# Performance work log

Hardware: AMD Instinct MI355X
Metric: run time of the kernel (lower is better)

## Reference

```python
import jax, jax.numpy as jnp
import numpy as np

B, S, D, H = 4, 2048, 512, 8
HD = D // H  # 64


def setup_inputs() -> dict:
    key = jax.random.key(0)
    ks = jax.random.split(key, 7)
    scale = 1.0 / np.sqrt(D)
    return {
        "query": jax.random.normal(ks[0], (B, S, D), jnp.float32),
        "key": jax.random.normal(ks[1], (B, S, D), jnp.float32),
        "value": jax.random.normal(ks[2], (B, S, D), jnp.float32),
        # Only the `query` Linear and fc_out are actually used in the original forward
        "Wq": jax.random.uniform(ks[3], (D, D), jnp.float32, -scale, scale),
        "bq": jnp.zeros((D,), jnp.float32),
        "Wo": jax.random.uniform(ks[4], (D, D), jnp.float32, -scale, scale),
        "bo": jnp.zeros((D,), jnp.float32),
    }


def reference(query, key, value, Wq, bq, Wo, bo):
    # Faithful to source: Q, K, V all use the *query* projection (bug preserved)
    def proj(x):
        # [B,S,D] -> [B,H,S,HD]
        y = x @ Wq + bq
        return y.reshape(B, S, H, HD).transpose(0, 2, 1, 3)

    Q, K, V = proj(query), proj(key), proj(value)
    scores = jnp.einsum("bhqd,bhkd->bhqk", Q, K) / jnp.sqrt(jnp.float32(HD))
    attn = jax.nn.softmax(scores, axis=-1)
    x = jnp.einsum("bhqk,bhkd->bhqd", attn, V)
    x = x.transpose(0, 2, 1, 3).reshape(B, S, D)
    return x @ Wo + bo
```

## Files before the change

### kernel.cpp

```cpp
#include <hip/hip_runtime.h>
#include <math.h>

#define B_ 4
#define S_ 2048
#define D_ 512
#define H_ 8
#define HD_ 64
#define SZ_ (B_ * S_ * D_)
#define WSZ_ (D_ * D_)
#define BSH_ (B_ * S_ * H_)

#define QSCALE_ 0.18033688011112042f

typedef _Float16 v4h __attribute__((ext_vector_type(4)));
typedef _Float16 v8h __attribute__((ext_vector_type(8)));
typedef float    v4f __attribute__((ext_vector_type(4)));

#define GLD16(g, l)                                                         \
    __builtin_amdgcn_global_load_lds(                                       \
        (const __attribute__((address_space(1))) unsigned int*)(g),         \
        (__attribute__((address_space(3))) unsigned int*)(l), 16, 0, 0)

__global__ __launch_bounds__(256) void wtrans_kernel(const float* __restrict__ Wq,
                                                     const float* __restrict__ Wo,
                                                     _Float16* __restrict__ Wt) {
    __shared__ float Ts[64][65];
    const float* W = blockIdx.z ? Wo : Wq;
    _Float16* dst = Wt + (size_t)blockIdx.z * WSZ_;
    const int t = threadIdx.x;
    const int k0 = blockIdx.y * 64, n0 = blockIdx.x * 64;
#pragma unroll
    for (int i = 0; i < 4; i++) {
        int c = t + i * 256;
        int kk = c >> 4, nc = (c & 15) * 4;
        float4 w = *(const float4*)&W[(size_t)(k0 + kk) * 512 + n0 + nc];
        Ts[nc + 0][kk] = w.x;
        Ts[nc + 1][kk] = w.y;
        Ts[nc + 2][kk] = w.z;
        Ts[nc + 3][kk] = w.w;
    }
    __syncthreads();
#pragma unroll
    for (int i = 0; i < 2; i++) {
        int c = t + i * 256;
        int n = c >> 3, kc = (c & 7) * 8;
        v8h p;
#pragma unroll
        for (int j = 0; j < 8; j++) p[j] = (_Float16)Ts[n][kc + j];
        *(v8h*)&dst[(size_t)(n0 + n) * 512 + k0 + kc] = p;
    }
}

__global__ __launch_bounds__(256) void proj_mfma(const float* __restrict__ q,
                                                 const float* __restrict__ k,
                                                 const float* __restrict__ v,
                                                 const _Float16* __restrict__ Wt,
                                                 const float* __restrict__ bq,
                                                 _Float16* __restrict__ Qh,
                                                 _Float16* __restrict__ Kh,
                                                 _Float16* __restrict__ VT) {
    __shared__ _Float16 As[128 * 32];
    __shared__ _Float16 Bs[128 * 32];
    const int z  = blockIdx.z;
    const float* X = (z == 0) ? q : ((z == 1) ? k : v);
    const int n0 = blockIdx.x * 128, m0 = blockIdx.y * 128;
    const int t    = threadIdx.x;
    const int lane = t & 63;
    const int w    = t >> 6;
    const int wm   = w >> 1, wn = w & 1;
    const int quad = lane >> 4, l16 = lane & 15;

    v4f acc[4][4];
#pragma unroll
    for (int mi = 0; mi < 4; mi++)
#pragma unroll
        for (int ni = 0; ni < 4; ni++) acc[mi][ni] = (v4f)0.f;

    const int s0 = t, s1 = t + 256;
    const int r0 = s0 >> 2, c0 = (s0 & 3) * 8;
    const int r1 = s1 >> 2, c1 = (s1 & 3) * 8;
    const float* A0 = X + (size_t)(m0 + r0) * 512 + c0;
    const float* A1 = X + (size_t)(m0 + r1) * 512 + c1;
    const _Float16* B0 = Wt + (size_t)(n0 + r0) * 512 + c0;
    const _Float16* B1 = Wt + (size_t)(n0 + r1) * 512 + c1;

    for (int k0 = 0; k0 < 512; k0 += 32) {
        v4f a00 = *(const v4f*)(A0 + k0);
        v4f a01 = *(const v4f*)(A0 + k0 + 4);
        v4f a10 = *(const v4f*)(A1 + k0);
        v4f a11 = *(const v4f*)(A1 + k0 + 4);
        __syncthreads();
        GLD16(B0 + k0, &Bs[s0 * 8]);
        GLD16(B1 + k0, &Bs[s1 * 8]);
        v4h p0lo = __builtin_convertvector(a00, v4h);
        v4h p0hi = __builtin_convertvector(a01, v4h);
        v4h p1lo = __builtin_convertvector(a10, v4h);
        v4h p1hi = __builtin_convertvector(a11, v4h);
        *(v8h*)&As[s0 * 8] = __builtin_shufflevector(p0lo, p0hi, 0, 1, 2, 3, 4, 5, 6, 7);
        *(v8h*)&As[s1 * 8] = __builtin_shufflevector(p1lo, p1hi, 0, 1, 2, 3, 4, 5, 6, 7);
        __syncthreads();

        v8h af[4], bf[4];
#pragma unroll
        for (int mi = 0; mi < 4; mi++)
            af[mi] = *(const v8h*)&As[(wm * 64 + mi * 16 + l16) * 32 + quad * 8];
#pragma unroll
        for (int ni = 0; ni < 4; ni++)
            bf[ni] = *(const v8h*)&Bs[(wn * 64 + ni * 16 + l16) * 32 + quad * 8];
#pragma unroll
        for (int mi = 0; mi < 4; mi++)
#pragma unroll
            for (int ni = 0; ni < 4; ni++)
                acc[mi][ni] = __builtin_amdgcn_mfma_f32_16x16x32_f16(af[mi], bf[ni], acc[mi][ni], 0, 0, 0);
    }

    if (z < 2) {
        _Float16* Y = z ? Kh : Qh;
        const float sc = z ? 1.f : QSCALE_;
#pragma unroll
        for (int mi = 0; mi < 4; mi++) {
            int mb = m0 + wm * 64 + mi * 16 + quad * 4;
#pragma unroll
            for (int ni = 0; ni < 4; ni++) {
                int n = n0 + wn * 64 + ni * 16 + l16;
                float bj = bq[n];
#pragma unroll
                for (int r = 0; r < 4; r++)
                    Y[(size_t)(mb + r) * 512 + n] = (_Float16)((acc[mi][ni][r] + bj) * sc);
            }
        }
    } else {
#pragma unroll
        for (int mi = 0; mi < 4; mi++) {
            int tile0 = (m0 & 2047) + wm * 64;
            int pos = tile0 + (mi >> 1) * 32 + quad * 8 + (mi & 1) * 4;
            int b = m0 >> 11;
#pragma unroll
            for (int ni = 0; ni < 4; ni++) {
                int n = n0 + wn * 64 + ni * 16 + l16;
                int h = n >> 6, d = n & 63;
                float bj = bq[n];
                v4h pk;
#pragma unroll
                for (int r = 0; r < 4; r++) pk[r] = (_Float16)(acc[mi][ni][r] + bj);
                *(v4h*)&VT[(((size_t)b * H_ + h) * HD_ + d) * S_ + pos] = pk;
            }
        }
    }
}

__global__ __launch_bounds__(256) void outproj_mfma(const float* __restrict__ Op,
                                                    const float* __restrict__ lp,
                                                    const _Float16* __restrict__ Wt,
                                                    const float* __restrict__ bo,
                                                    float* __restrict__ out) {
    __shared__ _Float16 As[128 * 32];
    __shared__ _Float16 Bs[128 * 32];
    const int n0 = blockIdx.x * 128, m0 = blockIdx.y * 128;
    const int t    = threadIdx.x;
    const int lane = t & 63;
    const int w    = t >> 6;
    const int wm   = w >> 1, wn = w & 1;
    const int quad = lane >> 4, l16 = lane & 15;

    v4f acc[4][4];
#pragma unroll
    for (int mi = 0; mi < 4; mi++)
#pragma unroll
        for (int ni = 0; ni < 4; ni++) acc[mi][ni] = (v4f)0.f;

    const int s0 = t, s1 = t + 256;
    const int r0 = s0 >> 2, c0 = (s0 & 3) * 8;
    const int r1 = s1 >> 2, c1 = (s1 & 3) * 8;
    const float* O10 = Op + (size_t)(m0 + r0) * 512 + c0;
    const float* O11 = Op + (size_t)(m0 + r1) * 512 + c1;
    const float* O20 = O10 + SZ_;
    const float* O21 = O11 + SZ_;
    const float* lp10 = lp + (size_t)(m0 + r0) * H_;
    const float* lp11 = lp + (size_t)(m0 + r1) * H_;
    const _Float16* B0 = Wt + (size_t)WSZ_ + (size_t)(n0 + r0) * 512 + c0;
    const _Float16* B1 = Wt + (size_t)WSZ_ + (size_t)(n0 + r1) * 512 + c1;

    for (int k0 = 0; k0 < 512; k0 += 32) {
        const int hh = k0 >> 6;
        v4f a00 = *(const v4f*)(O10 + k0);
        v4f a01 = *(const v4f*)(O10 + k0 + 4);
        v4f a10 = *(const v4f*)(O11 + k0);
        v4f a11 = *(const v4f*)(O11 + k0 + 4);
        v4f b00 = *(const v4f*)(O20 + k0);
        v4f b01 = *(const v4f*)(O20 + k0 + 4);
        v4f b10 = *(const v4f*)(O21 + k0);
        v4f b11 = *(const v4f*)(O21 + k0 + 4);
        float linv0 = __builtin_amdgcn_rcpf(lp10[hh] + lp10[BSH_ + hh]);
        float linv1 = __builtin_amdgcn_rcpf(lp11[hh] + lp11[BSH_ + hh]);
        __syncthreads();
        GLD16(B0 + k0, &Bs[s0 * 8]);
        GLD16(B1 + k0, &Bs[s1 * 8]);
        v4f s0a = (a00 + b00) * linv0, s0b = (a01 + b01) * linv0;
        v4f s1a = (a10 + b10) * linv1, s1b = (a11 + b11) * linv1;
        v4h p0lo = __builtin_convertvector(s0a, v4h);
        v4h p0hi = __builtin_convertvector(s0b, v4h);
        v4h p1lo = __builtin_convertvector(s1a, v4h);
        v4h p1hi = __builtin_convertvector(s1b, v4h);
        *(v8h*)&As[s0 * 8] = __builtin_shufflevector(p0lo, p0hi, 0, 1, 2, 3, 4, 5, 6, 7);
        *(v8h*)&As[s1 * 8] = __builtin_shufflevector(p1lo, p1hi, 0, 1, 2, 3, 4, 5, 6, 7);
        __syncthreads();

        v8h af[4], bf[4];
#pragma unroll
        for (int mi = 0; mi < 4; mi++)
            af[mi] = *(const v8h*)&As[(wm * 64 + mi * 16 + l16) * 32 + quad * 8];
#pragma unroll
        for (int ni = 0; ni < 4; ni++)
            bf[ni] = *(const v8h*)&Bs[(wn * 64 + ni * 16 + l16) * 32 + quad * 8];
#pragma unroll
        for (int mi = 0; mi < 4; mi++)
#pragma unroll
            for (int ni = 0; ni < 4; ni++)
                acc[mi][ni] = __builtin_amdgcn_mfma_f32_16x16x32_f16(af[mi], bf[ni], acc[mi][ni], 0, 0, 0);
    }

#pragma unroll
    for (int mi = 0; mi < 4; mi++) {
        int mb = m0 + wm * 64 + mi * 16 + quad * 4;
#pragma unroll
        for (int ni = 0; ni < 4; ni++) {
            int n = n0 + wn * 64 + ni * 16 + l16;
            float bj = bo[n];
#pragma unroll
            for (int r = 0; r < 4; r++)
                out[(size_t)(mb + r) * 512 + n] = acc[mi][ni][r] + bj;
        }
    }
}

__global__ __launch_bounds__(256) void flash_attn_f16(const _Float16* __restrict__ Qh,
                                                      const _Float16* __restrict__ Kh,
                                                      const _Float16* __restrict__ VT,
                                                      float* __restrict__ Op,
                                                      float* __restrict__ lp) {
    __shared__ _Float16 Ks[128 * 72];
    __shared__ _Float16 Vs[64 * 136];

    const int t     = threadIdx.x;
    const int lane  = t & 63;
    const int w     = t >> 6;
    const int quad  = lane >> 4;
    const int l16   = lane & 15;
    const int q0    = blockIdx.x * 128;
    const int h     = blockIdx.y;
    const int b     = blockIdx.z >> 1;
    const int split = blockIdx.z & 1;

    const size_t base  = (size_t)b * S_ * D_ + (size_t)h * HD_;
    const size_t vbase = ((size_t)b * H_ + h) * HD_ * (size_t)S_;

    v8h qf[2][2];
#pragma unroll
    for (int nb = 0; nb < 2; nb++) {
        const _Float16* qrow = Qh + base + (size_t)(q0 + w * 32 + nb * 16 + l16) * D_;
        qf[nb][0] = *(const v8h*)(qrow + quad * 8);
        qf[nb][1] = *(const v8h*)(qrow + 32 + quad * 8);
    }

    v4f o[2][4];
#pragma unroll
    for (int nb = 0; nb < 2; nb++)
#pragma unroll
        for (int i = 0; i < 4; i++) o[nb][i] = (v4f)0.f;
    float l_lane[2] = {0.f, 0.f};

    const int kbeg = split * (S_ / 2);
    const int kend = kbeg + S_ / 2;

    v8h kv[4], vv[4];
#define LOADKV(kk)                                                             \
    do {                                                                       \
        _Pragma("unroll") for (int i = 0; i < 4; i++) {                        \
            int c = t + i * 256;                                               \
            kv[i] = *(const v8h*)(Kh + base + (size_t)((kk) + (c >> 3)) * D_ + (c & 7) * 8); \
            vv[i] = *(const v8h*)(VT + vbase + (size_t)(c >> 4) * S_ + (kk) + (c & 15) * 8); \
        }                                                                      \
    } while (0)

    LOADKV(kbeg);

    for (int kk0 = kbeg; kk0 < kend; kk0 += 128) {
        __syncthreads();
#pragma unroll
        for (int i = 0; i < 4; i++) {
            int c = t + i * 256;
            *(v8h*)&Ks[(c >> 3) * 72 + (c & 7) * 8] = kv[i];
            *(v8h*)&Vs[(c >> 4) * 136 + (c & 15) * 8] = vv[i];
        }
        __syncthreads();

        if (kk0 + 128 < kend) LOADKV(kk0 + 128);

#pragma unroll
        for (int hh = 0; hh < 2; hh++) {
            v4f sc[4][2];
#pragma unroll
            for (int mb = 0; mb < 4; mb++)
#pragma unroll
                for (int nb = 0; nb < 2; nb++) sc[mb][nb] = (v4f)0.f;
#pragma unroll
            for (int ks = 0; ks < 2; ks++) {
#pragma unroll
                for (int mb = 0; mb < 4; mb++) {
                    v8h ak = *(const v8h*)&Ks[(hh * 64 + mb * 16 + l16) * 72 + ks * 32 + quad * 8];
#pragma unroll
                    for (int nb = 0; nb < 2; nb++)
                        sc[mb][nb] = __builtin_amdgcn_mfma_f32_16x16x32_f16(ak, qf[nb][ks], sc[mb][nb], 0, 0, 0);
                }
            }

            v4h pf[4][2];
#pragma unroll
            for (int nb = 0; nb < 2; nb++) {
#pragma unroll
                for (int mb = 0; mb < 4; mb++) {
                    v4f pv;
#pragma unroll
                    for (int r = 0; r < 4; r++) pv[r] = __builtin_amdgcn_exp2f(sc[mb][nb][r]);
                    pf[mb][nb] = __builtin_convertvector(pv, v4h);
                    l_lane[nb] += (pv[0] + pv[1]) + (pv[2] + pv[3]);
                }
            }

#pragma unroll
            for (int p = 0; p < 2; p++) {
#pragma unroll
                for (int dblk = 0; dblk < 4; dblk++) {
                    v8h vf2 = *(const v8h*)&Vs[(dblk * 16 + l16) * 136 + hh * 64 + p * 32 + quad * 8];
                    v4h vlo = __builtin_shufflevector(vf2, vf2, 0, 1, 2, 3);
                    v4h vhi = __builtin_shufflevector(vf2, vf2, 4, 5, 6, 7);
#pragma unroll
                    for (int nb = 0; nb < 2; nb++) {
                        o[nb][dblk] = __builtin_amdgcn_mfma_f32_16x16x16f16(vlo, pf[2 * p][nb], o[nb][dblk], 0, 0, 0);
                        o[nb][dblk] = __builtin_amdgcn_mfma_f32_16x16x16f16(vhi, pf[2 * p + 1][nb], o[nb][dblk], 0, 0, 0);
                    }
                }
            }
        }
    }
#undef LOADKV

    float* Ops = Op + (size_t)split * SZ_;
#pragma unroll
    for (int nb = 0; nb < 2; nb++) {
        float rs = l_lane[nb];
        rs += __shfl_xor(rs, 16);
        rs += __shfl_xor(rs, 32);
        int qrow = q0 + w * 32 + nb * 16 + l16;
        if (quad == 0)
            lp[(size_t)split * BSH_ + ((size_t)b * S_ + qrow) * H_ + h] = rs;
        const size_t rbase = base + (size_t)qrow * D_;
#pragma unroll
        for (int dblk = 0; dblk < 4; dblk++)
            *(v4f*)&Ops[rbase + dblk * 16 + quad * 4] = o[nb][dblk];
    }
}

extern "C" void kernel_launch(void* const* d_in, const int* in_sizes, int n_in,
                              void* d_out, int out_size, void* d_ws, size_t ws_size,
                              hipStream_t stream) {
    const float* query = (const float*)d_in[0];
    const float* key   = (const float*)d_in[1];
    const float* value = (const float*)d_in[2];
    const float* Wq    = (const float*)d_in[3];
    const float* bq    = (const float*)d_in[4];
    const float* Wo    = (const float*)d_in[5];
    const float* bo    = (const float*)d_in[6];
    float* out = (float*)d_out;

    _Float16* ws = (_Float16*)d_ws;
    _Float16* Qh = ws;
    _Float16* Kh = ws + (size_t)SZ_;
    _Float16* VT = ws + 2 * (size_t)SZ_;
    _Float16* Wt = ws + 3 * (size_t)SZ_;
    float*    Op = (float*)(ws + 3 * (size_t)SZ_ + 2 * (size_t)WSZ_);
    float*    lp = Op + 2 * (size_t)SZ_;

    wtrans_kernel<<<dim3(8, 8, 2), 256, 0, stream>>>(Wq, Wo, Wt);
    proj_mfma<<<dim3(4, 64, 3), 256, 0, stream>>>(query, key, value, Wt, bq, Qh, Kh, VT);
    flash_attn_f16<<<dim3(S_ / 128, H_, B_ * 2), 256, 0, stream>>>(Qh, Kh, VT, Op, lp);
    outproj_mfma<<<dim3(4, 64, 1), 256, 0, stream>>>(Op, lp, Wt, bo, out);
}
```

Measured before the change: 216.2 us.

## Register-prefetch next K tile and pad LDS rows in projection GEMMs

Both projection GEMM kernels now load the next K-slice of A and B into registers while the MFMAs for the current slice run, so global latency overlaps compute. The global_load_lds path for B is replaced by register loads followed by LDS stores. LDS rows are padded from 32 to 40 halfs to reduce bank conflicts on the fragment reads. The cost is more registers per thread and extra LDS store instructions.

```diff
diff --git a/kernel.cpp b/kernel.cpp
--- a/kernel.cpp
+++ b/kernel.cpp
@@ -16,11 +16,6 @@
 typedef _Float16 v8h __attribute__((ext_vector_type(8)));
 typedef float    v4f __attribute__((ext_vector_type(4)));
 
-#define GLD16(g, l)                                                         \
-    __builtin_amdgcn_global_load_lds(                                       \
-        (const __attribute__((address_space(1))) unsigned int*)(g),         \
-        (__attribute__((address_space(3))) unsigned int*)(l), 16, 0, 0)
-
 __global__ __launch_bounds__(256) void wtrans_kernel(const float* __restrict__ Wq,
                                                      const float* __restrict__ Wo,
                                                      _Float16* __restrict__ Wt) {
@@ -59,8 +54,8 @@
                                                  _Float16* __restrict__ Qh,
                                                  _Float16* __restrict__ Kh,
                                                  _Float16* __restrict__ VT) {
-    __shared__ _Float16 As[128 * 32];
-    __shared__ _Float16 Bs[128 * 32];
+    __shared__ _Float16 As[128 * 40];
+    __shared__ _Float16 Bs[128 * 40];
     const int z  = blockIdx.z;
     const float* X = (z == 0) ? q : ((z == 1) ? k : v);
     const int n0 = blockIdx.x * 128, m0 = blockIdx.y * 128;
@@ -84,29 +79,37 @@
     const _Float16* B0 = Wt + (size_t)(n0 + r0) * 512 + c0;
     const _Float16* B1 = Wt + (size_t)(n0 + r1) * 512 + c1;
 
+    v4f a00 = *(const v4f*)(A0 + 0), a01 = *(const v4f*)(A0 + 4);
+    v4f a10 = *(const v4f*)(A1 + 0), a11 = *(const v4f*)(A1 + 4);
+    v8h b0 = *(const v8h*)(B0 + 0), b1 = *(const v8h*)(B1 + 0);
+
     for (int k0 = 0; k0 < 512; k0 += 32) {
-        v4f a00 = *(const v4f*)(A0 + k0);
-        v4f a01 = *(const v4f*)(A0 + k0 + 4);
-        v4f a10 = *(const v4f*)(A1 + k0);
-        v4f a11 = *(const v4f*)(A1 + k0 + 4);
-        __syncthreads();
-        GLD16(B0 + k0, &Bs[s0 * 8]);
-        GLD16(B1 + k0, &Bs[s1 * 8]);
-        v4h p0lo = __builtin_convertvector(a00, v4h);
-        v4h p0hi = __builtin_convertvector(a01, v4h);
-        v4h p1lo = __builtin_convertvector(a10, v4h);
-        v4h p1hi = __builtin_convertvector(a11, v4h);
-        *(v8h*)&As[s0 * 8] = __builtin_shufflevector(p0lo, p0hi, 0, 1, 2, 3, 4, 5, 6, 7);
-        *(v8h*)&As[s1 * 8] = __builtin_shufflevector(p1lo, p1hi, 0, 1, 2, 3, 4, 5, 6, 7);
-        __syncthreads();
+        v8h af0 = __builtin_shufflevector(__builtin_convertvector(a00, v4h),
+                                          __builtin_convertvector(a01, v4h),
+                                          0, 1, 2, 3, 4, 5, 6, 7);
+        v8h af1 = __builtin_shufflevector(__builtin_convertvector(a10, v4h),
+                                          __builtin_convertvector(a11, v4h),
+                                          0, 1, 2, 3, 4, 5, 6, 7);
+        __syncthreads();
+        *(v8h*)&As[r0 * 40 + c0] = af0;
+        *(v8h*)&As[r1 * 40 + c1] = af1;
+        *(v8h*)&Bs[r0 * 40 + c0] = b0;
+        *(v8h*)&Bs[r1 * 40 + c1] = b1;
+        __syncthreads();
+
+        if (k0 + 32 < 512) {
+            a00 = *(const v4f*)(A0 + k0 + 32); a01 = *(const v4f*)(A0 + k0 + 36);
+            a10 = *(const v4f*)(A1 + k0 + 32); a11 = *(const v4f*)(A1 + k0 + 36);
+            b0 = *(const v8h*)(B0 + k0 + 32);  b1 = *(const v8h*)(B1 + k0 + 32);
+        }
 
         v8h af[4], bf[4];
 #pragma unroll
         for (int mi = 0; mi < 4; mi++)
-            af[mi] = *(const v8h*)&As[(wm * 64 + mi * 16 + l16) * 32 + quad * 8];
+            af[mi] = *(const v8h*)&As[(wm * 64 + mi * 16 + l16) * 40 + quad * 8];
 #pragma unroll
         for (int ni = 0; ni < 4; ni++)
-            bf[ni] = *(const v8h*)&Bs[(wn * 64 + ni * 16 + l16) * 32 + quad * 8];
+            bf[ni] = *(const v8h*)&Bs[(wn * 64 + ni * 16 + l16) * 40 + quad * 8];
 #pragma unroll
         for (int mi = 0; mi < 4; mi++)
 #pragma unroll
@@ -154,8 +157,8 @@
                                                     const _Float16* __restrict__ Wt,
                                                     const float* __restrict__ bo,
                                                     float* __restrict__ out) {
-    __shared__ _Float16 As[128 * 32];
-    __shared__ _Float16 Bs[128 * 32];
+    __shared__ _Float16 As[128 * 40];
+    __shared__ _Float16 Bs[128 * 40];
     const int n0 = blockIdx.x * 128, m0 = blockIdx.y * 128;
     const int t    = threadIdx.x;
     const int lane = t & 63;
@@ -176,43 +179,56 @@
     const float* O11 = Op + (size_t)(m0 + r1) * 512 + c1;
     const float* O20 = O10 + SZ_;
     const float* O21 = O11 + SZ_;
-    const float* lp10 = lp + (size_t)(m0 + r0) * H_;
-    const float* lp11 = lp + (size_t)(m0 + r1) * H_;
+    const float* lp0 = lp + (size_t)(m0 + r0) * H_;
+    const float* lp1 = lp + (size_t)(m0 + r1) * H_;
     const _Float16* B0 = Wt + (size_t)WSZ_ + (size_t)(n0 + r0) * 512 + c0;
     const _Float16* B1 = Wt + (size_t)WSZ_ + (size_t)(n0 + r1) * 512 + c1;
 
+    v4f a00 = *(const v4f*)(O10 + 0), a01 = *(const v4f*)(O10 + 4);
+    v4f a10 = *(const v4f*)(O11 + 0), a11 = *(const v4f*)(O11 + 4);
+    v4f c00 = *(const v4f*)(O20 + 0), c01 = *(const v4f*)(O20 + 4);
+    v4f c10 = *(const v4f*)(O21 + 0), c11 = *(const v4f*)(O21 + 4);
+    float lv0 = lp0[0] + lp0[BSH_], lv1 = lp1[0] + lp1[BSH_];
+    v8h b0 = *(const v8h*)(B0 + 0), b1 = *(const v8h*)(B1 + 0);
+
     for (int k0 = 0; k0 < 512; k0 += 32) {
-        const int hh = k0 >> 6;
-        v4f a00 = *(const v4f*)(O10 + k0);
-        v4f a01 = *(const v4f*)(O10 + k0 + 4);
-        v4f a10 = *(const v4f*)(O11 + k0);
-        v4f a11 = *(const v4f*)(O11 + k0 + 4);
-        v4f b00 = *(const v4f*)(O20 + k0);
-        v4f b01 = *(const v4f*)(O20 + k0 + 4);
-        v4f b10 = *(const v4f*)(O21 + k0);
-        v4f b11 = *(const v4f*)(O21 + k0 + 4);
-        float linv0 = __builtin_amdgcn_rcpf(lp10[hh] + lp10[BSH_ + hh]);
-        float linv1 = __builtin_amdgcn_rcpf(lp11[hh] + lp11[BSH_ + hh]);
-        __syncthreads();
-        GLD16(B0 + k0, &Bs[s0 * 8]);
-        GLD16(B1 + k0, &Bs[s1 * 8]);
-        v4f s0a = (a00 + b00) * linv0, s0b = (a01 + b01) * linv0;
-        v4f s1a = (a10 + b10) * linv1, s1b = (a11 + b11) * linv1;
-        v4h p0lo = __builtin_convertvector(s0a, v4h);
-        v4h p0hi = __builtin_convertvector(s0b, v4h);
-        v4h p1lo = __builtin_convertvector(s1a, v4h);
-        v4h p1hi = __builtin_convertvector(s1b, v4h);
-        *(v8h*)&As[s0 * 8] = __builtin_shufflevector(p0lo, p0hi, 0, 1, 2, 3, 4, 5, 6, 7);
-        *(v8h*)&As[s1 * 8] = __builtin_shufflevector(p1lo, p1hi, 0, 1, 2, 3, 4, 5, 6, 7);
-        __syncthreads();
+        float linv0 = __builtin_amdgcn_rcpf(lv0);
+        float linv1 = __builtin_amdgcn_rcpf(lv1);
+        v4f s0a = (a00 + c00) * linv0, s0b = (a01 + c01) * linv0;
+        v4f s1a = (a10 + c10) * linv1, s1b = (a11 + c11) * linv1;
+        v8h af0 = __builtin_shufflevector(__builtin_convertvector(s0a, v4h),
+                                          __builtin_convertvector(s0b, v4h),
+                                          0, 1, 2, 3, 4, 5, 6, 7);
+        v8h af1 = __builtin_shufflevector(__builtin_convertvector(s1a, v4h),
+                                          __builtin_convertvector(s1b, v4h),
+                                          0, 1, 2, 3, 4, 5, 6, 7);
+        __syncthreads();
+        *(v8h*)&As[r0 * 40 + c0] = af0;
+        *(v8h*)&As[r1 * 40 + c1] = af1;
+        *(v8h*)&Bs[r0 * 40 + c0] = b0;
+        *(v8h*)&Bs[r1 * 40 + c1] = b1;
+        __syncthreads();
+
+        if (k0 + 32 < 512) {
+            int kn = k0 + 32;
+            int hh = kn >> 6;
+            a00 = *(const v4f*)(O10 + kn); a01 = *(const v4f*)(O10 + kn + 4);
+            a10 = *(const v4f*)(O11 + kn); a11 = *(const v4f*)(O11 + kn + 4);
+            c00 = *(const v4f*)(O20 + kn); c01 = *(const v4f*)(O20 + kn + 4);
+            c10 = *(const v4f*)(O21 + kn); c11 = *(const v4f*)(O21 + kn + 4);
+            lv0 = lp0[hh] + lp0[BSH_ + hh];
+            lv1 = lp1[hh] + lp1[BSH_ + hh];
+            b0 = *(const v8h*)(B0 + kn);
+            b1 = *(const v8h*)(B1 + kn);
+        }
 
         v8h af[4], bf[4];
 #pragma unroll
         for (int mi = 0; mi < 4; mi++)
-            af[mi] = *(const v8h*)&As[(wm * 64 + mi * 16 + l16) * 32 + quad * 8];
+            af[mi] = *(const v8h*)&As[(wm * 64 + mi * 16 + l16) * 40 + quad * 8];
 #pragma unroll
         for (int ni = 0; ni < 4; ni++)
-            bf[ni] = *(const v8h*)&Bs[(wn * 64 + ni * 16 + l16) * 32 + quad * 8];
+            bf[ni] = *(const v8h*)&Bs[(wn * 64 + ni * 16 + l16) * 40 + quad * 8];
 #pragma unroll
         for (int mi = 0; mi < 4; mi++)
 #pragma unroll
```

Result: faster. 211.7 us (-2.1%).
